# Kernel tuning notes

Measured on AMD Instinct MI355X. Metric: run time of the kernel, lower is better.

The kernel has to match this reference:

```python
import jax, jax.numpy as jnp
import numpy as np

N, D = 20000, 16          # nodes, fixed in-degree
IN, HID, OUT = 128, 128, 1


def _lstm_final_h(x_seq, Wih, Whh, bih, bhh):
    # x_seq: [D, N, F]; LSTM with hidden size H == F, zero init state.
    # Returns final hidden state h_D: [N, H]. PyTorch gate order i,f,g,o.
    Nn = x_seq.shape[1]
    H = Whh.shape[1]
    b = bih + bhh

    def step(carry, xt):
        h, c = carry
        gates = xt @ Wih.T + h @ Whh.T + b          # [N, 4H]
        i, f, g, o = jnp.split(gates, 4, axis=-1)
        c = jax.nn.sigmoid(f) * c + jax.nn.sigmoid(i) * jnp.tanh(g)
        h = jax.nn.sigmoid(o) * jnp.tanh(c)
        return (h, c), None

    init = (jnp.zeros((Nn, H), x_seq.dtype), jnp.zeros((Nn, H), x_seq.dtype))
    (h, _), _ = jax.lax.scan(step, init, x_seq)
    return h


def _sage_lstm(x, nbr_idx, Wih, Whh, bih, bhh, Wself, Wneigh, bneigh):
    # DGL SAGEConv(aggregator='lstm'): out = fc_self(x) + fc_neigh(lstm(neighbors))
    msgs = x[nbr_idx]                                # gather: [N, D, F]
    hN = _lstm_final_h(jnp.swapaxes(msgs, 0, 1), Wih, Whh, bih, bhh)  # [N, F]
    return x @ Wself.T + hN @ Wneigh.T + bneigh


def setup_inputs() -> dict:
    key = jax.random.key(0)
    ks = jax.random.split(key, 16)
    s = 1.0 / float(np.sqrt(IN))
    u = lambda k, sh: jax.random.uniform(k, sh, jnp.float32, -s, s)
    return {
        "x": jax.random.normal(ks[0], (N, IN), jnp.float32),
        "nbr_idx": jax.random.randint(ks[1], (N, D), 0, N),
        "Wih1": u(ks[2], (4 * IN, IN)), "Whh1": u(ks[3], (4 * IN, IN)),
        "bih1": u(ks[4], (4 * IN,)), "bhh1": u(ks[5], (4 * IN,)),
        "Wself1": u(ks[6], (HID, IN)), "Wneigh1": u(ks[7], (HID, IN)),
        "bneigh1": jnp.zeros((HID,), jnp.float32),
        "Wih2": u(ks[8], (4 * HID, HID)), "Whh2": u(ks[9], (4 * HID, HID)),
        "bih2": u(ks[10], (4 * HID,)), "bhh2": u(ks[11], (4 * HID,)),
        "Wself2": u(ks[12], (OUT, HID)), "Wneigh2": u(ks[13], (OUT, HID)),
        "bneigh2": jnp.zeros((OUT,), jnp.float32),
    }


def reference(x, nbr_idx, Wih1, Whh1, bih1, bhh1, Wself1, Wneigh1, bneigh1,
              Wih2, Whh2, bih2, bhh2, Wself2, Wneigh2, bneigh2):
    h = _sage_lstm(x, nbr_idx, Wih1, Whh1, bih1, bhh1, Wself1, Wneigh1, bneigh1)
    h = jax.nn.relu(h)
    h = _sage_lstm(h, nbr_idx, Wih2, Whh2, bih2, bhh2, Wself2, Wneigh2, bneigh2)
    return jax.nn.sigmoid(h)
```

## Files before the change

### kernel.cpp

```cpp
#include <hip/hip_runtime.h>


#define NN   20000
#define L2E  1.4426950408889634f

typedef unsigned short u16;
typedef __attribute__((ext_vector_type(8))) short frag8;
typedef __attribute__((ext_vector_type(4))) float facc4;
typedef __attribute__((ext_vector_type(8))) _Float16 half8;

#define OFF_X16   0u
#define OFF_H1    5120000u
#define OFF_WIH1P 15360000u
#define OFF_WHH1P 15491072u
#define OFF_WIH2P 15622144u
#define OFF_WHH2P 15753216u
#define OFF_WS1P  15884288u
#define OFF_WN1P  15917056u
#define OFF_WS2B  15949824u
#define OFF_WN2B  15950080u
#define OFF_B1    15950336u
#define OFF_B2    15952384u
#define OFF_XPRE  15954432u

__device__ __forceinline__ u16 f2bf(float f) {
  union { float f; unsigned u; } v; v.f = f;
  unsigned r = (v.u + 0x7fffu + ((v.u >> 16) & 1u)) >> 16;
  return (u16)r;
}
__device__ __forceinline__ float bflo(unsigned u) {
  union { unsigned u; float f; } v; v.u = u << 16; return v.f;
}
__device__ __forceinline__ float bfhi(unsigned u) {
  union { unsigned u; float f; } v; v.u = u & 0xffff0000u; return v.f;
}
__device__ __forceinline__ unsigned pk2h(float a, float b) {
  union { _Float16 h[2]; unsigned u; } v;
  v.h[0] = (_Float16)a; v.h[1] = (_Float16)b;
  return v.u;
}
__device__ __forceinline__ unsigned pkbf(float a, float b) {
  unsigned r;
  asm("v_cvt_pk_bf16_f32 %0, %1, %2" : "=v"(r) : "v"(a), "v"(b));
  return r;
}
__device__ __forceinline__ facc4 mfma16(frag8 a, frag8 b, facc4 c) {
  return __builtin_amdgcn_mfma_f32_16x16x32_bf16(a, b, c, 0, 0, 0);
}
__device__ __forceinline__ float sigm_ps(float xp) {
  return __builtin_amdgcn_rcpf(1.f + __builtin_amdgcn_exp2f(-xp));
}
__device__ __forceinline__ float tanh_ps(float xp) {
  return 1.f - 2.f * __builtin_amdgcn_rcpf(1.f + __builtin_amdgcn_exp2f(xp));
}
__device__ __forceinline__ float gate_scale(int row) {
  return (row >= 256 && row < 384) ? 2.f * L2E : L2E;
}
__device__ __forceinline__ float dot2(unsigned a, unsigned b) {
  return bflo(a) * bflo(b) + bfhi(a) * bfhi(b);
}

__device__ __forceinline__ void pack512(u16* dst, const float* src, int i) {
  int e = i & 7, ln = (i >> 3) & 63, kb = (i >> 9) & 3, tj = i >> 11;
  int row = tj * 16 + (ln & 15);
  int col = kb * 32 + (ln >> 4) * 8 + e;
  dst[i] = f2bf(src[row * 128 + col] * gate_scale(row));
}
__device__ __forceinline__ void pack128(u16* dst, const float* src, int i) {
  int e = i & 7, ln = (i >> 3) & 63, kb = (i >> 9) & 3, tj = i >> 11;
  dst[i] = f2bf(src[(tj * 16 + (ln & 15)) * 128 + kb * 32 + (ln >> 4) * 8 + e]);
}

__global__ __launch_bounds__(256) void pack_kernel(
    const float* __restrict__ x,
    const float* __restrict__ Wih1, const float* __restrict__ Whh1,
    const float* __restrict__ bih1, const float* __restrict__ bhh1,
    const float* __restrict__ Wself1, const float* __restrict__ Wneigh1,
    const float* __restrict__ Wih2, const float* __restrict__ Whh2,
    const float* __restrict__ bih2, const float* __restrict__ bhh2,
    const float* __restrict__ Wself2, const float* __restrict__ Wneigh2,
    char* __restrict__ ws)
{
  int i = blockIdx.x * 256 + threadIdx.x;
  if (i < 640000) {
    float4 v = ((const float4*)x)[i];
    uint2 st = { pkbf(v.x, v.y), pkbf(v.z, v.w) };
    ((uint2*)(ws + OFF_X16))[i] = st;
    return;
  }
  i -= 640000;
  if (i < 65536) { pack512((u16*)(ws + OFF_WIH1P), Wih1, i); return; }
  i -= 65536;
  if (i < 65536) { pack512((u16*)(ws + OFF_WHH1P), Whh1, i); return; }
  i -= 65536;
  if (i < 65536) { pack512((u16*)(ws + OFF_WIH2P), Wih2, i); return; }
  i -= 65536;
  if (i < 65536) { pack512((u16*)(ws + OFF_WHH2P), Whh2, i); return; }
  i -= 65536;
  if (i < 16384) { pack128((u16*)(ws + OFF_WS1P), Wself1, i); return; }
  i -= 16384;
  if (i < 16384) { pack128((u16*)(ws + OFF_WN1P), Wneigh1, i); return; }
  i -= 16384;
  if (i < 128) { ((u16*)(ws + OFF_WS2B))[i] = f2bf(Wself2[i]); return; }
  i -= 128;
  if (i < 128) { ((u16*)(ws + OFF_WN2B))[i] = f2bf(Wneigh2[i]); return; }
  i -= 128;
  if (i < 512) { ((float*)(ws + OFF_B1))[i] = (bih1[i] + bhh1[i]) * gate_scale(i); return; }
  i -= 512;
  if (i < 512) { ((float*)(ws + OFF_B2))[i] = (bih2[i] + bhh2[i]) * gate_scale(i); }
}

__global__ __launch_bounds__(512) void xpre_kernel(
    const u16* __restrict__ inp,
    const frag8* __restrict__ Wp,
    const float* __restrict__ bias,
    u16* __restrict__ outp)
{
  __shared__ __align__(16) u16 stage[64][512];
  const int tid = threadIdx.x;
  const int lane = tid & 63, wave = tid >> 6;
  const int m = lane & 15, quad = lane >> 4;
  const int rg = wave & 3, jh = wave >> 2;
  const int row = blockIdx.x * 64 + rg * 16 + m;
  if (row < NN) {
    frag8 bfr[4];
#pragma unroll
    for (int kb = 0; kb < 4; ++kb)
      bfr[kb] = *(const frag8*)(inp + (size_t)row * 128 + kb * 32 + quad * 8);
    u16* srow = stage[rg * 16 + m];
#pragma unroll
    for (int j = 0; j < 16; ++j) {
      const int tj = jh * 16 + j;
      float4 bv = *(const float4*)(bias + tj * 16 + quad * 4);
      facc4 acc = {bv.x, bv.y, bv.z, bv.w};
#pragma unroll
      for (int kb = 0; kb < 4; ++kb)
        acc = mfma16(Wp[(tj * 4 + kb) * 64 + lane], bfr[kb], acc);
      uint2 st = { pk2h(acc[0], acc[1]), pk2h(acc[2], acc[3]) };
      *(uint2*)(srow + (tj & 7) * 64 + quad * 16 + (tj >> 3) * 4) = st;
    }
  }
  __syncthreads();
  const int base = blockIdx.x * 64;
#pragma unroll
  for (int i = tid; i < 4096; i += 512) {
    int r = i >> 6, cc = i & 63;
    int n = base + r;
    if (n < NN)
      ((uint4*)(outp + (size_t)n * 512))[cc] = ((const uint4*)stage[r])[cc];
  }
}

__global__ __launch_bounds__(512, 4) void lstm_kernel(
    const u16* __restrict__ Xpre,
    const frag8* __restrict__ Wp,
    const int* __restrict__ nbr,
    const u16* __restrict__ xin,
    const frag8* __restrict__ Wsp, const frag8* __restrict__ Wnp,
    const float* __restrict__ bias_o,
    const u16* __restrict__ ws2, const u16* __restrict__ wn2,
    const float* __restrict__ b2,
    u16* __restrict__ h1,
    float* __restrict__ outp,
    int mode)
{
  __shared__ __align__(16) u16 h_lds[2][16 * 136];
  const int tid = threadIdx.x;
  const int lane = tid & 63, g = tid >> 6;
  const int m = lane & 15, quad = lane >> 4;

  frag8 A[4][4];
#pragma unroll
  for (int gate = 0; gate < 4; ++gate)
#pragma unroll
    for (int kb = 0; kb < 4; ++kb)
      A[gate][kb] = Wp[((gate * 8 + g) * 4 + kb) * 64 + lane];

  for (int i = tid; i < 16 * 136; i += 512) h_lds[0][i] = 0;

  const int node_base = blockIdx.x * 16;
  int4 idx4 = *(const int4*)(nbr + (size_t)(node_base + m) * 16 + quad * 4);

  facc4 c = {0.f, 0.f, 0.f, 0.f};

  auto xslice = [&](int t) -> const uint4* {
    const int tq = t >> 2, ts = t & 3;
    int sel = (ts == 0) ? idx4.x : (ts == 1) ? idx4.y : (ts == 2) ? idx4.z : idx4.w;
    int idx = __shfl(sel, m + (tq << 4), 64);
    return (const uint4*)(Xpre + (size_t)idx * 512) + g * 8 + quad * 2;
  };

  uint4 pX0, pX1;
  { const uint4* p0 = xslice(0); pX0 = p0[0]; pX1 = p0[1]; }

  __syncthreads();

#pragma unroll 1
  for (int t = 0; t < 16; ++t) {
    const u16* hr = h_lds[t & 1];
    u16* hw = h_lds[(t + 1) & 1];
    const uint4* pn = xslice(t < 15 ? t + 1 : 15);

    frag8 bfr[4];
#pragma unroll
    for (int kb = 0; kb < 4; ++kb)
      bfr[kb] = *(const frag8*)(hr + m * 136 + kb * 32 + quad * 8);

    union { uint4 u; half8 h; } ua, ub;
    ua.u = pX0; ub.u = pX1;
    facc4 ai = {(float)ua.h[0], (float)ua.h[1], (float)ua.h[2], (float)ua.h[3]};
    facc4 af = {(float)ua.h[4], (float)ua.h[5], (float)ua.h[6], (float)ua.h[7]};
    facc4 ag = {(float)ub.h[0], (float)ub.h[1], (float)ub.h[2], (float)ub.h[3]};
    facc4 ao = {(float)ub.h[4], (float)ub.h[5], (float)ub.h[6], (float)ub.h[7]};
    pX0 = pn[0]; pX1 = pn[1];

#pragma unroll
    for (int kb = 0; kb < 4; ++kb) {
      ai = mfma16(A[0][kb], bfr[kb], ai);
      af = mfma16(A[1][kb], bfr[kb], af);
      ag = mfma16(A[2][kb], bfr[kb], ag);
      ao = mfma16(A[3][kb], bfr[kb], ao);
    }

    facc4 hv;
#pragma unroll
    for (int r = 0; r < 4; ++r) {
      float si = sigm_ps(ai[r]);
      float sf = sigm_ps(af[r]);
      float tg = tanh_ps(ag[r]);
      float cn = sf * c[r] + si * tg;
      c[r] = cn;
      float so = sigm_ps(ao[r]);
      hv[r] = so * tanh_ps((2.f * L2E) * cn);
    }
    uint2 hp = { pkbf(hv[0], hv[1]), pkbf(hv[2], hv[3]) };
    *(uint2*)(hw + m * 136 + g * 16 + quad * 4) = hp;
    asm volatile("s_waitcnt lgkmcnt(0)" ::: "memory");
    __builtin_amdgcn_s_barrier();
  }

  const u16* hf = h_lds[0];

  if (mode == 0) {
    const int row = node_base + m;
    frag8 bx[4], bh[4];
#pragma unroll
    for (int kb = 0; kb < 4; ++kb) {
      bx[kb] = *(const frag8*)(xin + (size_t)row * 128 + kb * 32 + quad * 8);
      bh[kb] = *(const frag8*)(hf + m * 136 + kb * 32 + quad * 8);
    }
    float4 bv = *(const float4*)(bias_o + g * 16 + quad * 4);
    facc4 acc = {bv.x, bv.y, bv.z, bv.w};
#pragma unroll
    for (int kb = 0; kb < 4; ++kb) {
      frag8 wsk = Wsp[(g * 4 + kb) * 64 + lane];
      acc = mfma16(wsk, bx[kb], acc);
      frag8 wnk = Wnp[(g * 4 + kb) * 64 + lane];
      acc = mfma16(wnk, bh[kb], acc);
    }
    uint2 st = { pkbf(fmaxf(acc[0], 0.f), fmaxf(acc[1], 0.f)),
                 pkbf(fmaxf(acc[2], 0.f), fmaxf(acc[3], 0.f)) };
    u16* stg = (u16*)h_lds[1];
    *(uint2*)(stg + m * 136 + g * 16 + quad * 4) = st;
    __syncthreads();
    const int r = tid >> 5, cc = tid & 31;
    *(uint2*)(h1 + (size_t)(node_base + r) * 128 + cc * 4) =
        *(const uint2*)(stg + r * 136 + cc * 4);
  } else {
    const int n = tid >> 5, cc = tid & 31;
    uint2 a = *(const uint2*)(h1 + (size_t)(node_base + n) * 128 + cc * 4);
    uint2 w = *(const uint2*)(ws2 + cc * 4);
    uint2 b = *(const uint2*)(hf + n * 136 + cc * 4);
    uint2 v = *(const uint2*)(wn2 + cc * 4);
    float p = dot2(a.x, w.x) + dot2(a.y, w.y) + dot2(b.x, v.x) + dot2(b.y, v.y);
#pragma unroll
    for (int s = 1; s < 32; s <<= 1) p += __shfl_xor(p, s, 64);
    if (cc == 0) {
      float acc = p + b2[0];
      outp[node_base + n] =
          __builtin_amdgcn_rcpf(1.f + __builtin_amdgcn_exp2f(-acc * L2E));
    }
  }
}

extern "C" void kernel_launch(void* const* d_in, const int* in_sizes, int n_in,
                              void* d_out, int out_size, void* d_ws, size_t ws_size,
                              hipStream_t stream) {
  const float* x       = (const float*)d_in[0];
  const int*   nbr     = (const int*)d_in[1];
  const float* Wih1    = (const float*)d_in[2];
  const float* Whh1    = (const float*)d_in[3];
  const float* bih1    = (const float*)d_in[4];
  const float* bhh1    = (const float*)d_in[5];
  const float* Wself1  = (const float*)d_in[6];
  const float* Wneigh1 = (const float*)d_in[7];
  const float* bneigh1 = (const float*)d_in[8];
  const float* Wih2    = (const float*)d_in[9];
  const float* Whh2    = (const float*)d_in[10];
  const float* bih2    = (const float*)d_in[11];
  const float* bhh2    = (const float*)d_in[12];
  const float* Wself2  = (const float*)d_in[13];
  const float* Wneigh2 = (const float*)d_in[14];
  const float* bneigh2 = (const float*)d_in[15];

  char* ws = (char*)d_ws;
  u16*   x16   = (u16*)(ws + OFF_X16);
  u16*   h1    = (u16*)(ws + OFF_H1);
  u16*   Xpre  = (u16*)(ws + OFF_XPRE);
  frag8* Wih1p = (frag8*)(ws + OFF_WIH1P);
  frag8* Whh1p = (frag8*)(ws + OFF_WHH1P);
  frag8* Wih2p = (frag8*)(ws + OFF_WIH2P);
  frag8* Whh2p = (frag8*)(ws + OFF_WHH2P);
  frag8* Ws1p  = (frag8*)(ws + OFF_WS1P);
  frag8* Wn1p  = (frag8*)(ws + OFF_WN1P);
  u16*   Ws2b  = (u16*)(ws + OFF_WS2B);
  u16*   Wn2b  = (u16*)(ws + OFF_WN2B);
  float* b1    = (float*)(ws + OFF_B1);
  float* b2    = (float*)(ws + OFF_B2);

  pack_kernel<<<3657, 256, 0, stream>>>(x, Wih1, Whh1, bih1, bhh1, Wself1,
                                        Wneigh1, Wih2, Whh2, bih2, bhh2,
                                        Wself2, Wneigh2, ws);
  xpre_kernel<<<313, 512, 0, stream>>>(x16, Wih1p, b1, Xpre);
  lstm_kernel<<<1250, 512, 0, stream>>>(Xpre, Whh1p, nbr, x16, Ws1p, Wn1p,
                                        bneigh1, Ws2b, Wn2b, bneigh2, h1,
                                        (float*)d_out, 0);
  xpre_kernel<<<313, 512, 0, stream>>>(h1, Wih2p, b2, Xpre);
  lstm_kernel<<<1250, 512, 0, stream>>>(Xpre, Whh2p, nbr, x16, Ws1p, Wn1p,
                                        bneigh1, Ws2b, Wn2b, bneigh2, h1,
                                        (float*)d_out, 1);
}
```

Baseline: 258.2 us.

## Fuse layer-2 input projection into layer-1 LSTM epilogue and x conversion into prep

Folds the bf16 conversion of x into the first input-projection kernel, which now writes both x16 and the projected gates in one pass, and drops the separate x-packing work from pack_kernel. The layer-1 LSTM epilogue now multiplies the freshly computed h1 tile by Wih2 and writes the layer-2 pre-activations straight to a second buffer, so the standalone xpre launch between the two LSTM kernels goes away. The aim is fewer launches and no re-read of x16 and h1 from global memory. In exchange, the layer-1 LSTM kernel uses more LDS and holds more registers in its epilogue, which may lower occupancy, and the workspace grows to hold two Xpre buffers.

```diff
diff --git a/kernel.cpp b/kernel.cpp
--- a/kernel.cpp
+++ b/kernel.cpp
@@ -21,7 +21,8 @@
 #define OFF_WN2B  15950080u
 #define OFF_B1    15950336u
 #define OFF_B2    15952384u
-#define OFF_XPRE  15954432u
+#define OFF_XPREA 15954432u
+#define OFF_XPREB 36434432u
 
 __device__ __forceinline__ u16 f2bf(float f) {
   union { float f; unsigned u; } v; v.f = f;
@@ -72,7 +73,6 @@
 }
 
 __global__ __launch_bounds__(256) void pack_kernel(
-    const float* __restrict__ x,
     const float* __restrict__ Wih1, const float* __restrict__ Whh1,
     const float* __restrict__ bih1, const float* __restrict__ bhh1,
     const float* __restrict__ Wself1, const float* __restrict__ Wneigh1,
@@ -82,13 +82,6 @@
     char* __restrict__ ws)
 {
   int i = blockIdx.x * 256 + threadIdx.x;
-  if (i < 640000) {
-    float4 v = ((const float4*)x)[i];
-    uint2 st = { pkbf(v.x, v.y), pkbf(v.z, v.w) };
-    ((uint2*)(ws + OFF_X16))[i] = st;
-    return;
-  }
-  i -= 640000;
   if (i < 65536) { pack512((u16*)(ws + OFF_WIH1P), Wih1, i); return; }
   i -= 65536;
   if (i < 65536) { pack512((u16*)(ws + OFF_WHH1P), Whh1, i); return; }
@@ -110,44 +103,54 @@
   if (i < 512) { ((float*)(ws + OFF_B2))[i] = (bih2[i] + bhh2[i]) * gate_scale(i); }
 }
 
-__global__ __launch_bounds__(512) void xpre_kernel(
-    const u16* __restrict__ inp,
+__global__ __launch_bounds__(512) void prep1_kernel(
+    const float* __restrict__ x,
     const frag8* __restrict__ Wp,
     const float* __restrict__ bias,
-    u16* __restrict__ outp)
+    u16* __restrict__ x16,
+    u16* __restrict__ xpre)
 {
-  __shared__ __align__(16) u16 stage[64][512];
+  __shared__ __align__(16) u16 xt[32 * 136];
+  __shared__ __align__(16) u16 stage[32 * 520];
   const int tid = threadIdx.x;
+  const int base = blockIdx.x * 32;
+  {
+    int r = tid >> 4, o = (tid & 15) * 8;
+    const float* src = x + (size_t)(base + r) * 128 + o;
+    float4 v0 = *(const float4*)(src);
+    float4 v1 = *(const float4*)(src + 4);
+    uint4 st = { pkbf(v0.x, v0.y), pkbf(v0.z, v0.w),
+                 pkbf(v1.x, v1.y), pkbf(v1.z, v1.w) };
+    *(uint4*)(xt + r * 136 + o) = st;
+    *(uint4*)(x16 + (size_t)(base + r) * 128 + o) = st;
+  }
+  __syncthreads();
   const int lane = tid & 63, wave = tid >> 6;
   const int m = lane & 15, quad = lane >> 4;
-  const int rg = wave & 3, jh = wave >> 2;
-  const int row = blockIdx.x * 64 + rg * 16 + m;
-  if (row < NN) {
-    frag8 bfr[4];
+  const int rg = wave & 1, jh = wave >> 1;
+  const int r = rg * 16 + m;
+  frag8 bfr[4];
+#pragma unroll
+  for (int kb = 0; kb < 4; ++kb)
+    bfr[kb] = *(const frag8*)(xt + r * 136 + kb * 32 + quad * 8);
+  u16* srow = stage + r * 520;
+#pragma unroll
+  for (int j = 0; j < 8; ++j) {
+    const int tj = jh * 8 + j;
+    float4 bv = *(const float4*)(bias + tj * 16 + quad * 4);
+    facc4 acc = {bv.x, bv.y, bv.z, bv.w};
 #pragma unroll
     for (int kb = 0; kb < 4; ++kb)
-      bfr[kb] = *(const frag8*)(inp + (size_t)row * 128 + kb * 32 + quad * 8);
-    u16* srow = stage[rg * 16 + m];
-#pragma unroll
-    for (int j = 0; j < 16; ++j) {
-      const int tj = jh * 16 + j;
-      float4 bv = *(const float4*)(bias + tj * 16 + quad * 4);
-      facc4 acc = {bv.x, bv.y, bv.z, bv.w};
-#pragma unroll
-      for (int kb = 0; kb < 4; ++kb)
-        acc = mfma16(Wp[(tj * 4 + kb) * 64 + lane], bfr[kb], acc);
-      uint2 st = { pk2h(acc[0], acc[1]), pk2h(acc[2], acc[3]) };
-      *(uint2*)(srow + (tj & 7) * 64 + quad * 16 + (tj >> 3) * 4) = st;
-    }
+      acc = mfma16(Wp[(tj * 4 + kb) * 64 + lane], bfr[kb], acc);
+    uint2 st = { pk2h(acc[0], acc[1]), pk2h(acc[2], acc[3]) };
+    *(uint2*)(srow + (tj & 7) * 64 + quad * 16 + (tj >> 3) * 4) = st;
   }
   __syncthreads();
-  const int base = blockIdx.x * 64;
-#pragma unroll
-  for (int i = tid; i < 4096; i += 512) {
-    int r = i >> 6, cc = i & 63;
-    int n = base + r;
-    if (n < NN)
-      ((uint4*)(outp + (size_t)n * 512))[cc] = ((const uint4*)stage[r])[cc];
+#pragma unroll
+  for (int i = tid; i < 2048; i += 512) {
+    int rr = i >> 6, cc = i & 63;
+    ((uint4*)(xpre + (size_t)(base + rr) * 512))[cc] =
+        ((const uint4*)(stage + rr * 520))[cc];
   }
 }
 
@@ -158,13 +161,16 @@
     const u16* __restrict__ xin,
     const frag8* __restrict__ Wsp, const frag8* __restrict__ Wnp,
     const float* __restrict__ bias_o,
+    const frag8* __restrict__ WihX, const float* __restrict__ biasX,
+    u16* __restrict__ xpreOut,
     const u16* __restrict__ ws2, const u16* __restrict__ wn2,
-    const float* __restrict__ b2,
+    const float* __restrict__ b2o,
     u16* __restrict__ h1,
     float* __restrict__ outp,
     int mode)
 {
   __shared__ __align__(16) u16 h_lds[2][16 * 136];
+  __shared__ __align__(16) u16 xstage[16 * 520];
   const int tid = threadIdx.x;
   const int lane = tid & 63, g = tid >> 6;
   const int m = lane & 15, quad = lane >> 4;
@@ -263,9 +269,33 @@
     u16* stg = (u16*)h_lds[1];
     *(uint2*)(stg + m * 136 + g * 16 + quad * 4) = st;
     __syncthreads();
-    const int r = tid >> 5, cc = tid & 31;
-    *(uint2*)(h1 + (size_t)(node_base + r) * 128 + cc * 4) =
-        *(const uint2*)(stg + r * 136 + cc * 4);
+    {
+      const int r = tid >> 5, cc = tid & 31;
+      *(uint2*)(h1 + (size_t)(node_base + r) * 128 + cc * 4) =
+          *(const uint2*)(stg + r * 136 + cc * 4);
+    }
+    frag8 b2f[4];
+#pragma unroll
+    for (int kb = 0; kb < 4; ++kb)
+      b2f[kb] = *(const frag8*)(stg + m * 136 + kb * 32 + quad * 8);
+#pragma unroll
+    for (int j = 0; j < 4; ++j) {
+      const int tj = g * 4 + j;
+      float4 bx2 = *(const float4*)(biasX + tj * 16 + quad * 4);
+      facc4 acc2 = {bx2.x, bx2.y, bx2.z, bx2.w};
+#pragma unroll
+      for (int kb = 0; kb < 4; ++kb)
+        acc2 = mfma16(WihX[(tj * 4 + kb) * 64 + lane], b2f[kb], acc2);
+      uint2 st2 = { pk2h(acc2[0], acc2[1]), pk2h(acc2[2], acc2[3]) };
+      *(uint2*)(xstage + m * 520 + (tj & 7) * 64 + quad * 16 + (tj >> 3) * 4) = st2;
+    }
+    __syncthreads();
+#pragma unroll
+    for (int i = tid; i < 1024; i += 512) {
+      int rr = i >> 6, cc = i & 63;
+      ((uint4*)(xpreOut + (size_t)(node_base + rr) * 512))[cc] =
+          ((const uint4*)(xstage + rr * 520))[cc];
+    }
   } else {
     const int n = tid >> 5, cc = tid & 31;
     uint2 a = *(const uint2*)(h1 + (size_t)(node_base + n) * 128 + cc * 4);
@@ -276,7 +306,7 @@
 #pragma unroll
     for (int s = 1; s < 32; s <<= 1) p += __shfl_xor(p, s, 64);
     if (cc == 0) {
-      float acc = p + b2[0];
+      float acc = p + b2o[0];
       outp[node_base + n] =
           __builtin_amdgcn_rcpf(1.f + __builtin_amdgcn_exp2f(-acc * L2E));
     }
@@ -306,7 +336,8 @@
   char* ws = (char*)d_ws;
   u16*   x16   = (u16*)(ws + OFF_X16);
   u16*   h1    = (u16*)(ws + OFF_H1);
-  u16*   Xpre  = (u16*)(ws + OFF_XPRE);
+  u16*   XpreA = (u16*)(ws + OFF_XPREA);
+  u16*   XpreB = (u16*)(ws + OFF_XPREB);
   frag8* Wih1p = (frag8*)(ws + OFF_WIH1P);
   frag8* Whh1p = (frag8*)(ws + OFF_WHH1P);
   frag8* Wih2p = (frag8*)(ws + OFF_WIH2P);
@@ -318,15 +349,16 @@
   float* b1    = (float*)(ws + OFF_B1);
   float* b2    = (float*)(ws + OFF_B2);
 
-  pack_kernel<<<3657, 256, 0, stream>>>(x, Wih1, Whh1, bih1, bhh1, Wself1,
+  pack_kernel<<<1157, 256, 0, stream>>>(Wih1, Whh1, bih1, bhh1, Wself1,
                                         Wneigh1, Wih2, Whh2, bih2, bhh2,
                                         Wself2, Wneigh2, ws);
-  xpre_kernel<<<313, 512, 0, stream>>>(x16, Wih1p, b1, Xpre);
-  lstm_kernel<<<1250, 512, 0, stream>>>(Xpre, Whh1p, nbr, x16, Ws1p, Wn1p,
-                                        bneigh1, Ws2b, Wn2b, bneigh2, h1,
+  prep1_kernel<<<625, 512, 0, stream>>>(x, Wih1p, b1, x16, XpreA);
+  lstm_kernel<<<1250, 512, 0, stream>>>(XpreA, Whh1p, nbr, x16, Ws1p, Wn1p,
+                                        bneigh1, Wih2p, b2, XpreB,
+                                        Ws2b, Wn2b, bneigh2, h1,
                                         (float*)d_out, 0);
-  xpre_kernel<<<313, 512, 0, stream>>>(h1, Wih2p, b2, Xpre);
-  lstm_kernel<<<1250, 512, 0, stream>>>(Xpre, Whh2p, nbr, x16, Ws1p, Wn1p,
-                                        bneigh1, Ws2b, Wn2b, bneigh2, h1,
+  lstm_kernel<<<1250, 512, 0, stream>>>(XpreB, Whh2p, nbr, x16, Ws1p, Wn1p,
+                                        bneigh1, Wih2p, b2, XpreB,
+                                        Ws2b, Wn2b, bneigh2, h1,
                                         (float*)d_out, 1);
 }
```

Measured after the change: 245.5 us. 4.9% less time.
